# Kernel optimization log

Measured on AMD Instinct MI355X. Metric: run time of the kernel, lower is better.

The kernel has to match this reference:

```python
import jax, jax.numpy as jnp
import numpy as np


def setup_inputs() -> dict:
    key = jax.random.key(0)
    kq, kk, kv = jax.random.split(key, 3)
    B, S, D = 4, 4096, 128
    return {
        "q_proj": jax.random.normal(kq, (B, S, D), dtype=jnp.float32),
        "k_proj": jax.random.normal(kk, (B, S, D), dtype=jnp.float32),
        "v_proj": jax.random.normal(kv, (B, S, D), dtype=jnp.float32),
    }


def reference(q_proj, k_proj, v_proj):
    # Block-wise online softmax in the original is mathematically exact
    # full (non-causal) scaled dot-product attention.
    d = q_proj.shape[-1]
    scale = 1.0 / jnp.sqrt(jnp.asarray(d, dtype=q_proj.dtype))
    logits = jnp.einsum('bqd,bkd->bqk', q_proj, k_proj) * scale  # [B,S,S]
    attn = jax.nn.softmax(logits, axis=-1)
    return jnp.einsum('bqk,bkd->bqd', attn, v_proj)
```

## Files before the change

kernel.cpp:

```cpp
#include <hip/hip_runtime.h>
#include <hip/hip_bf16.h>
#include <stdint.h>

#define Bn 4
#define Sn 4096
#define Dn 128
#define SCALE ((float)(0.08838834764831843 * 1.4426950408889634))

typedef __attribute__((ext_vector_type(8)))  short short8;
typedef __attribute__((ext_vector_type(4)))  short short4v;
typedef __attribute__((ext_vector_type(4)))  float f32x4;
typedef __attribute__((ext_vector_type(16))) float f32x16;
typedef __attribute__((ext_vector_type(2)))  uint32_t uint2v;

__device__ __forceinline__ uint32_t bfround(float f){
  union { float f; uint32_t u; } a; a.f = f;
  return a.u + 0x7FFFu + ((a.u >> 16) & 1u);
}
__device__ __forceinline__ uint32_t f2bf2(float lo, float hi){
  return (bfround(hi) & 0xFFFF0000u) | (bfround(lo) >> 16);
}
__device__ __forceinline__ uint32_t f2bf2_fast(float lo, float hi){
  const uint32_t a = __float_as_uint(lo) + 0x8000u;
  const uint32_t b = __float_as_uint(hi) + 0x8000u;
  return __builtin_amdgcn_perm(b, a, 0x07060302u);
}
__device__ __forceinline__ float bf2f(short s){
  union { uint32_t u; float f; } a; a.u = ((uint32_t)(unsigned short)s) << 16; return a.f;
}
__device__ __forceinline__ float fexp2(float x){
#if __has_builtin(__builtin_amdgcn_exp2f)
  return __builtin_amdgcn_exp2f(x);
#else
  return exp2f(x);
#endif
}

__global__ void prep_kernel(const float* __restrict__ k, const float* __restrict__ v,
                            short* __restrict__ kb, short* __restrict__ vf){
  const int bid = blockIdx.x;
  const int t   = threadIdx.x;
  if (bid < 512){
    const int b = bid >> 7, i = bid & 127;
#pragma unroll
    for (int it=0; it<2; ++it){
      const int lin = it*256 + t;
      const int ln = lin & 31;
      const int tg = lin >> 5;
      const int tt = tg >> 1, hh = tg & 1;
      const float* src = k + ((size_t)(b*Sn + i*32 + ln))*Dn + tg*8;
      const f32x4 a = *(const f32x4*)src;
      const f32x4 c = *(const f32x4*)(src + 4);
      union { uint32_t u[4]; short8 s; } pk;
      pk.u[0] = f2bf2(a[0], a[1]);
      pk.u[1] = f2bf2(a[2], a[3]);
      pk.u[2] = f2bf2(c[0], c[1]);
      pk.u[3] = f2bf2(c[2], c[3]);
      *(short8*)(kb + (((size_t)(b*128 + i)*8 + tt)*64 + (hh*32 + ln))*8) = pk.s;
    }
  } else {
    __shared__ float tile[32][132];
    const int vb = bid - 512;
    const int b = vb >> 7, i = vb & 127;
#pragma unroll
    for (int it=0; it<4; ++it){
      const int lin = it*256 + t;
      const int row = lin >> 5;
      const int c4  = lin & 31;
      const f32x4 val = *(const f32x4*)(v + ((size_t)(b*Sn + i*32 + row))*Dn + c4*4);
      tile[row][c4*4+0] = val[0];
      tile[row][c4*4+1] = val[1];
      tile[row][c4*4+2] = val[2];
      tile[row][c4*4+3] = val[3];
    }
    __syncthreads();
#pragma unroll
    for (int cc=0; cc<2; ++cc){
      const int c = cc*256 + t;
      const int l = c & 63, fidx = c >> 6;
      const int t_ = fidx >> 2, mt = fidx & 3;
      const int ln = l & 31, h5 = l >> 5;
      const int d = mt*32 + ln;
      const int kb0 = 16*t_ + 4*h5;
      union { uint32_t u[4]; short8 s; } pk;
#pragma unroll
      for (int p=0;p<4;++p){
        const int j0 = 2*p, j1 = 2*p+1;
        const int kl0 = kb0 + (j0&3) + 8*(j0>>2);
        const int kl1 = kb0 + (j1&3) + 8*(j1>>2);
        pk.u[p] = f2bf2(tile[kl0][d], tile[kl1][d]);
      }
      *(short8*)(vf + (((size_t)(b*128 + i)*8 + fidx)*64 + l)*8) = pk.s;
    }
  }
}

__global__ __launch_bounds__(256, 2) void fa_kernel(
    const float* __restrict__ Qg, const short* __restrict__ Kb,
    const short* __restrict__ VFb, short* __restrict__ parts,
    float* __restrict__ lparts){
  const int tid = threadIdx.x;
  const int w = tid >> 6, lane = tid & 63;
  const int ln = lane & 31, h5 = lane >> 5;
  const int idx = blockIdx.x;
  const int b   = idx & 3;
  const int u2  = idx >> 2;
  const int qt  = u2 & 31;
  const int ks  = u2 >> 5;
  const int q0  = qt * 128;
  const int start_it = ks * 32;
  const int n_it     = 32;

  short8 Qf[8];
  {
    const float* qp = Qg + ((size_t)(b*Sn + q0 + w*32 + ln))*Dn;
#pragma unroll
    for (int t=0;t<8;++t){
      const int d0 = t*16 + h5*8;
      const f32x4 a = *(const f32x4*)(qp + d0);
      const f32x4 c = *(const f32x4*)(qp + d0 + 4);
      union { uint32_t u[4]; short8 s; } pk;
      pk.u[0] = f2bf2(a[0]*SCALE, a[1]*SCALE);
      pk.u[1] = f2bf2(a[2]*SCALE, a[3]*SCALE);
      pk.u[2] = f2bf2(c[0]*SCALE, c[1]*SCALE);
      pk.u[3] = f2bf2(c[2]*SCALE, c[3]*SCALE);
      Qf[t] = pk.s;
    }
  }

  f32x16 Ot[4];
#pragma unroll
  for (int m=0;m<4;++m)
#pragma unroll
    for (int r=0;r<16;++r) Ot[m][r] = 0.0f;
  float ls0=0.f, ls1=0.f, ls2=0.f, ls3=0.f;

  const short* Kbase = Kb  + (size_t)(b*128 + start_it)*4096 + (size_t)lane*8;
  const short* Vbase = VFb + (size_t)(b*128 + start_it)*4096 + (size_t)lane*8;

  short8 kf[8], vf[8];
  {
#pragma unroll
    for (int t=0;t<8;++t) kf[t] = *(const short8*)(Kbase + t*512);
#pragma unroll
    for (int t=0;t<8;++t) vf[t] = *(const short8*)(Vbase + t*512);
  }

  for (int i=0; i<n_it; ++i){
    f32x16 St;
#pragma unroll
    for (int r=0;r<16;++r) St[r] = 0.0f;
    __builtin_amdgcn_s_setprio(1);
#pragma unroll
    for (int t=0;t<8;++t)
      St = __builtin_amdgcn_mfma_f32_32x32x16_bf16(kf[t], Qf[t], St, 0, 0, 0);
    __builtin_amdgcn_s_setprio(0);

    {
      const short* Kp = Kbase + (size_t)(i+1)*4096;
#pragma unroll
      for (int t=0;t<8;++t) kf[t] = *(const short8*)(Kp + t*512);
    }
    __builtin_amdgcn_sched_barrier(0);

#pragma unroll
    for (int r=0;r<16;++r) St[r] = fexp2(St[r]);
#pragma unroll
    for (int r=0;r<16;r+=4){
      ls0 += St[r]; ls1 += St[r+1]; ls2 += St[r+2]; ls3 += St[r+3];
    }

    union { uint32_t u[4]; short8 s; } pf0, pf1;
    pf0.u[0] = f2bf2_fast(St[0], St[1]);
    pf0.u[1] = f2bf2_fast(St[2], St[3]);
    pf0.u[2] = f2bf2_fast(St[4], St[5]);
    pf0.u[3] = f2bf2_fast(St[6], St[7]);
    pf1.u[0] = f2bf2_fast(St[8], St[9]);
    pf1.u[1] = f2bf2_fast(St[10], St[11]);
    pf1.u[2] = f2bf2_fast(St[12], St[13]);
    pf1.u[3] = f2bf2_fast(St[14], St[15]);

    __builtin_amdgcn_s_setprio(1);
#pragma unroll
    for (int mt=0;mt<4;++mt)
      Ot[mt] = __builtin_amdgcn_mfma_f32_32x32x16_bf16(vf[mt],   pf0.s, Ot[mt], 0, 0, 0);
#pragma unroll
    for (int mt=0;mt<4;++mt)
      Ot[mt] = __builtin_amdgcn_mfma_f32_32x32x16_bf16(vf[4+mt], pf1.s, Ot[mt], 0, 0, 0);
    __builtin_amdgcn_s_setprio(0);

    {
      const short* Vp = Vbase + (size_t)(i+1)*4096;
#pragma unroll
      for (int t=0;t<8;++t) vf[t] = *(const short8*)(Vp + t*512);
    }
    __builtin_amdgcn_sched_barrier(0);
  }

  float lsum = (ls0 + ls1) + (ls2 + ls3);
  lsum += __shfl_xor(lsum, 32, 64);

  const int pslot = (b*32 + qt)*4 + ks;
  short* pbase = parts + (size_t)pslot*16384 + (size_t)(w*32 + ln)*128;
#pragma unroll
  for (int mt=0;mt<4;++mt){
#pragma unroll
    for (int g=0;g<4;++g){
      union { uint32_t u[2]; short4v s; } o;
      o.u[0] = f2bf2(Ot[mt][4*g],   Ot[mt][4*g+1]);
      o.u[1] = f2bf2(Ot[mt][4*g+2], Ot[mt][4*g+3]);
      *(short4v*)(pbase + mt*32 + 8*g + 4*h5) = o.s;
    }
  }
  if (h5 == 0) lparts[(size_t)pslot*128 + w*32 + ln] = lsum;
}

__global__ void reduce_kernel(const short* __restrict__ parts,
                              const float* __restrict__ lparts,
                              float* __restrict__ out){
  const int t  = threadIdx.x;
  const int s  = blockIdx.x >> 3;
  const int qg = (blockIdx.x & 7)*16 + (t >> 4);
  const int d0 = (t & 15) * 8;
  float acc[8];
#pragma unroll
  for (int j=0;j<8;++j) acc[j] = 0.0f;
  float lsum = 0.0f;
#pragma unroll
  for (int ks=0;ks<4;++ks){
    const short8 p = *(const short8*)(parts + ((size_t)(s*4+ks))*16384 + (size_t)qg*128 + d0);
#pragma unroll
    for (int j=0;j<8;++j) acc[j] += bf2f(p[j]);
    lsum += lparts[(size_t)(s*4+ks)*128 + qg];
  }
  const float linv = 1.0f / lsum;
  f32x4 o0, o1;
#pragma unroll
  for (int j=0;j<4;++j){ o0[j] = acc[j]*linv; o1[j] = acc[4+j]*linv; }
  float* op = out + ((size_t)(s*128 + qg))*128 + d0;
  *(f32x4*)op = o0;
  *(f32x4*)(op + 4) = o1;
}

extern "C" void kernel_launch(void* const* d_in, const int* in_sizes, int n_in,
                              void* d_out, int out_size, void* d_ws, size_t ws_size,
                              hipStream_t stream){
  const float* q = (const float*)d_in[0];
  const float* k = (const float*)d_in[1];
  const float* v = (const float*)d_in[2];
  float* out = (float*)d_out;
  char* ws = (char*)d_ws;
  short* kb     = (short*)ws;
  short* vfb    = kb + (size_t)Bn*Sn*Dn;
  short* parts  = (short*)(ws + 8388608);
  float* lparts = (float*)(ws + 8388608 + 16777216);

  prep_kernel<<<1024, 256, 0, stream>>>(k, v, kb, vfb);
  fa_kernel<<<512, 256, 0, stream>>>(q, kb, vfb, parts, lparts);
  reduce_kernel<<<1024, 256, 0, stream>>>(parts, lparts, out);
}
```

Measured before the change: 122.7 us.

## Software-pipeline QK^T MFMA one tile ahead of exp and PV

Restructures the attention loop so the QK^T scores for the next key tile are computed while the current tile's exponentials and PV MFMAs run, using two ping-ponged score accumulators. It also adds a prologue and epilogue, removes the sched_barrier and setprio hints, and prefetches K two tiles ahead. The aim is to overlap transcendental VALU work with matrix-core work within a wave. The cost is a second 16-float accumulator, which raises register pressure at 2 waves per SIMD, and the compiler's scheduling may now differ.

```diff
diff --git a/kernel.cpp b/kernel.cpp
--- a/kernel.cpp
+++ b/kernel.cpp
@@ -109,7 +109,6 @@
   const int ks  = u2 >> 5;
   const int q0  = qt * 128;
   const int start_it = ks * 32;
-  const int n_it     = 32;
 
   short8 Qf[8];
   {
@@ -135,66 +134,93 @@
     for (int r=0;r<16;++r) Ot[m][r] = 0.0f;
   float ls0=0.f, ls1=0.f, ls2=0.f, ls3=0.f;
 
+  f32x16 Zv;
+#pragma unroll
+  for (int r=0;r<16;++r) Zv[r] = 0.0f;
+
   const short* Kbase = Kb  + (size_t)(b*128 + start_it)*4096 + (size_t)lane*8;
   const short* Vbase = VFb + (size_t)(b*128 + start_it)*4096 + (size_t)lane*8;
 
   short8 kf[8], vf[8];
-  {
-#pragma unroll
-    for (int t=0;t<8;++t) kf[t] = *(const short8*)(Kbase + t*512);
-#pragma unroll
-    for (int t=0;t<8;++t) vf[t] = *(const short8*)(Vbase + t*512);
-  }
-
-  for (int i=0; i<n_it; ++i){
-    f32x16 St;
-#pragma unroll
-    for (int r=0;r<16;++r) St[r] = 0.0f;
-    __builtin_amdgcn_s_setprio(1);
-#pragma unroll
-    for (int t=0;t<8;++t)
-      St = __builtin_amdgcn_mfma_f32_32x32x16_bf16(kf[t], Qf[t], St, 0, 0, 0);
-    __builtin_amdgcn_s_setprio(0);
-
+#pragma unroll
+  for (int t=0;t<8;++t) kf[t] = *(const short8*)(Kbase + t*512);
+#pragma unroll
+  for (int t=0;t<8;++t) vf[t] = *(const short8*)(Vbase + t*512);
+
+  f32x16 StA, StB;
+  StA = __builtin_amdgcn_mfma_f32_32x32x16_bf16(kf[0], Qf[0], Zv, 0, 0, 0);
+#pragma unroll
+  for (int t=1;t<8;++t)
+    StA = __builtin_amdgcn_mfma_f32_32x32x16_bf16(kf[t], Qf[t], StA, 0, 0, 0);
+#pragma unroll
+  for (int t=0;t<8;++t) kf[t] = *(const short8*)(Kbase + 4096 + t*512);
+
+  auto body = [&](int i, f32x16& Scur, f32x16& Snx) {
+    Snx = __builtin_amdgcn_mfma_f32_32x32x16_bf16(kf[0], Qf[0], Zv, 0, 0, 0);
+#pragma unroll
+    for (int t=1;t<8;++t)
+      Snx = __builtin_amdgcn_mfma_f32_32x32x16_bf16(kf[t], Qf[t], Snx, 0, 0, 0);
     {
-      const short* Kp = Kbase + (size_t)(i+1)*4096;
+      const short* Kp = Kbase + (size_t)(i+2)*4096;
 #pragma unroll
       for (int t=0;t<8;++t) kf[t] = *(const short8*)(Kp + t*512);
     }
-    __builtin_amdgcn_sched_barrier(0);
-
-#pragma unroll
-    for (int r=0;r<16;++r) St[r] = fexp2(St[r]);
+#pragma unroll
+    for (int r=0;r<16;++r) Scur[r] = fexp2(Scur[r]);
 #pragma unroll
     for (int r=0;r<16;r+=4){
-      ls0 += St[r]; ls1 += St[r+1]; ls2 += St[r+2]; ls3 += St[r+3];
-    }
-
+      ls0 += Scur[r]; ls1 += Scur[r+1]; ls2 += Scur[r+2]; ls3 += Scur[r+3];
+    }
     union { uint32_t u[4]; short8 s; } pf0, pf1;
-    pf0.u[0] = f2bf2_fast(St[0], St[1]);
-    pf0.u[1] = f2bf2_fast(St[2], St[3]);
-    pf0.u[2] = f2bf2_fast(St[4], St[5]);
-    pf0.u[3] = f2bf2_fast(St[6], St[7]);
-    pf1.u[0] = f2bf2_fast(St[8], St[9]);
-    pf1.u[1] = f2bf2_fast(St[10], St[11]);
-    pf1.u[2] = f2bf2_fast(St[12], St[13]);
-    pf1.u[3] = f2bf2_fast(St[14], St[15]);
-
-    __builtin_amdgcn_s_setprio(1);
+    pf0.u[0] = f2bf2_fast(Scur[0],  Scur[1]);
+    pf0.u[1] = f2bf2_fast(Scur[2],  Scur[3]);
+    pf0.u[2] = f2bf2_fast(Scur[4],  Scur[5]);
+    pf0.u[3] = f2bf2_fast(Scur[6],  Scur[7]);
+    pf1.u[0] = f2bf2_fast(Scur[8],  Scur[9]);
+    pf1.u[1] = f2bf2_fast(Scur[10], Scur[11]);
+    pf1.u[2] = f2bf2_fast(Scur[12], Scur[13]);
+    pf1.u[3] = f2bf2_fast(Scur[14], Scur[15]);
 #pragma unroll
     for (int mt=0;mt<4;++mt)
       Ot[mt] = __builtin_amdgcn_mfma_f32_32x32x16_bf16(vf[mt],   pf0.s, Ot[mt], 0, 0, 0);
 #pragma unroll
     for (int mt=0;mt<4;++mt)
       Ot[mt] = __builtin_amdgcn_mfma_f32_32x32x16_bf16(vf[4+mt], pf1.s, Ot[mt], 0, 0, 0);
-    __builtin_amdgcn_s_setprio(0);
-
     {
       const short* Vp = Vbase + (size_t)(i+1)*4096;
 #pragma unroll
       for (int t=0;t<8;++t) vf[t] = *(const short8*)(Vp + t*512);
     }
-    __builtin_amdgcn_sched_barrier(0);
+  };
+
+  for (int i=0; i<30; i+=2){
+    body(i,   StA, StB);
+    body(i+1, StB, StA);
+  }
+  body(30, StA, StB);
+
+  {
+#pragma unroll
+    for (int r=0;r<16;++r) StB[r] = fexp2(StB[r]);
+#pragma unroll
+    for (int r=0;r<16;r+=4){
+      ls0 += StB[r]; ls1 += StB[r+1]; ls2 += StB[r+2]; ls3 += StB[r+3];
+    }
+    union { uint32_t u[4]; short8 s; } pf0, pf1;
+    pf0.u[0] = f2bf2_fast(StB[0],  StB[1]);
+    pf0.u[1] = f2bf2_fast(StB[2],  StB[3]);
+    pf0.u[2] = f2bf2_fast(StB[4],  StB[5]);
+    pf0.u[3] = f2bf2_fast(StB[6],  StB[7]);
+    pf1.u[0] = f2bf2_fast(StB[8],  StB[9]);
+    pf1.u[1] = f2bf2_fast(StB[10], StB[11]);
+    pf1.u[2] = f2bf2_fast(StB[12], StB[13]);
+    pf1.u[3] = f2bf2_fast(StB[14], StB[15]);
+#pragma unroll
+    for (int mt=0;mt<4;++mt)
+      Ot[mt] = __builtin_amdgcn_mfma_f32_32x32x16_bf16(vf[mt],   pf0.s, Ot[mt], 0, 0, 0);
+#pragma unroll
+    for (int mt=0;mt<4;++mt)
+      Ot[mt] = __builtin_amdgcn_mfma_f32_32x32x16_bf16(vf[4+mt], pf1.s, Ot[mt], 0, 0, 0);
   }
 
   float lsum = (ls0 + ls1) + (ls2 + ls3);
```

Result: no change. 124.1 us (+1.1%).

## Stage K/V tiles in LDS via async global-to-LDS loads, two Q tiles per wave

Applied to the files above, without the earlier changes.

Each block now has two waves, and each wave owns two 32-row Q tiles. The waves cooperatively stream K and V blocks into double-buffered shared memory with global_load_lds, so each K/V fragment is read from LDS once and reused across two MFMA accumulators. The key dimension is split six ways instead of four (768 blocks), and the reduce kernel and workspace offsets are updated to match. This cuts per-wave global K/V traffic and raises MFMA density per load. In exchange it adds a __syncthreads per iteration, more accumulator registers, and uneven split lengths.

```diff
diff --git a/kernel.cpp b/kernel.cpp
--- a/kernel.cpp
+++ b/kernel.cpp
@@ -34,6 +34,12 @@
 #else
   return exp2f(x);
 #endif
+}
+
+__device__ __forceinline__ void gload16(const void* g, void* l){
+  __builtin_amdgcn_global_load_lds(
+      (const __attribute__((address_space(1))) unsigned int*)g,
+      (__attribute__((address_space(3))) unsigned int*)l, 16, 0, 0);
 }
 
 __global__ void prep_kernel(const float* __restrict__ k, const float* __restrict__ v,
@@ -95,10 +101,11 @@
   }
 }
 
-__global__ __launch_bounds__(256, 2) void fa_kernel(
+__global__ __launch_bounds__(128, 2) void fa_kernel(
     const float* __restrict__ Qg, const short* __restrict__ Kb,
     const short* __restrict__ VFb, short* __restrict__ parts,
     float* __restrict__ lparts){
+  __shared__ __align__(16) char lds[32768];
   const int tid = threadIdx.x;
   const int w = tid >> 6, lane = tid & 63;
   const int ln = lane & 31, h5 = lane >> 5;
@@ -108,12 +115,13 @@
   const int qt  = u2 & 31;
   const int ks  = u2 >> 5;
   const int q0  = qt * 128;
-  const int start_it = ks * 32;
-  const int n_it     = 32;
-
-  short8 Qf[8];
-  {
-    const float* qp = Qg + ((size_t)(b*Sn + q0 + w*32 + ln))*Dn;
+  const int start_it = ks*21 + (ks < 2 ? ks : 2);
+  const int n_it     = 21 + (ks < 2 ? 1 : 0);
+
+  short8 Qf[2][8];
+#pragma unroll
+  for (int tile=0;tile<2;++tile){
+    const float* qp = Qg + ((size_t)(b*Sn + q0 + w*64 + tile*32 + ln))*Dn;
 #pragma unroll
     for (int t=0;t<8;++t){
       const int d0 = t*16 + h5*8;
@@ -124,95 +132,108 @@
       pk.u[1] = f2bf2(a[2]*SCALE, a[3]*SCALE);
       pk.u[2] = f2bf2(c[0]*SCALE, c[1]*SCALE);
       pk.u[3] = f2bf2(c[2]*SCALE, c[3]*SCALE);
-      Qf[t] = pk.s;
-    }
-  }
-
-  f32x16 Ot[4];
-#pragma unroll
-  for (int m=0;m<4;++m)
-#pragma unroll
-    for (int r=0;r<16;++r) Ot[m][r] = 0.0f;
-  float ls0=0.f, ls1=0.f, ls2=0.f, ls3=0.f;
-
-  const short* Kbase = Kb  + (size_t)(b*128 + start_it)*4096 + (size_t)lane*8;
-  const short* Vbase = VFb + (size_t)(b*128 + start_it)*4096 + (size_t)lane*8;
-
-  short8 kf[8], vf[8];
-  {
-#pragma unroll
-    for (int t=0;t<8;++t) kf[t] = *(const short8*)(Kbase + t*512);
-#pragma unroll
-    for (int t=0;t<8;++t) vf[t] = *(const short8*)(Vbase + t*512);
-  }
+      Qf[tile][t] = pk.s;
+    }
+  }
+
+  f32x16 Ot[2][4];
+#pragma unroll
+  for (int tile=0;tile<2;++tile)
+#pragma unroll
+    for (int m=0;m<4;++m)
+#pragma unroll
+      for (int r=0;r<16;++r) Ot[tile][m][r] = 0.0f;
+  float ls00=0.f, ls01=0.f, ls10=0.f, ls11=0.f;
+
+  const char* gsrc0 = (w ? (const char*)VFb : (const char*)Kb)
+                    + (size_t)(b*128)*8192 + (size_t)lane*16;
+  auto stage = [&](int it, int ph){
+    char* dst = lds + ph*16384 + (w ? 8192 : 0);
+    const char* src = gsrc0 + (size_t)it*8192;
+#pragma unroll
+    for (int u=0;u<8;++u) gload16(src + u*1024, dst + u*1024);
+  };
+
+  stage(start_it, 0);
 
   for (int i=0; i<n_it; ++i){
-    f32x16 St;
-#pragma unroll
-    for (int r=0;r<16;++r) St[r] = 0.0f;
+    const int ph = i & 1;
+    __syncthreads();
+    if (i+1 < n_it) stage(start_it+i+1, ph^1);
+
+    const char* bK = lds + ph*16384 + (size_t)lane*16;
+    const char* bV = bK + 8192;
+
+    f32x16 St0, St1;
+#pragma unroll
+    for (int r=0;r<16;++r){ St0[r] = 0.0f; St1[r] = 0.0f; }
     __builtin_amdgcn_s_setprio(1);
 #pragma unroll
-    for (int t=0;t<8;++t)
-      St = __builtin_amdgcn_mfma_f32_32x32x16_bf16(kf[t], Qf[t], St, 0, 0, 0);
+    for (int t=0;t<8;++t){
+      const short8 kf = *(const short8*)(bK + t*1024);
+      St0 = __builtin_amdgcn_mfma_f32_32x32x16_bf16(kf, Qf[0][t], St0, 0, 0, 0);
+      St1 = __builtin_amdgcn_mfma_f32_32x32x16_bf16(kf, Qf[1][t], St1, 0, 0, 0);
+    }
     __builtin_amdgcn_s_setprio(0);
 
-    {
-      const short* Kp = Kbase + (size_t)(i+1)*4096;
-#pragma unroll
-      for (int t=0;t<8;++t) kf[t] = *(const short8*)(Kp + t*512);
-    }
-    __builtin_amdgcn_sched_barrier(0);
-
-#pragma unroll
-    for (int r=0;r<16;++r) St[r] = fexp2(St[r]);
-#pragma unroll
-    for (int r=0;r<16;r+=4){
-      ls0 += St[r]; ls1 += St[r+1]; ls2 += St[r+2]; ls3 += St[r+3];
-    }
-
-    union { uint32_t u[4]; short8 s; } pf0, pf1;
-    pf0.u[0] = f2bf2_fast(St[0], St[1]);
-    pf0.u[1] = f2bf2_fast(St[2], St[3]);
-    pf0.u[2] = f2bf2_fast(St[4], St[5]);
-    pf0.u[3] = f2bf2_fast(St[6], St[7]);
-    pf1.u[0] = f2bf2_fast(St[8], St[9]);
-    pf1.u[1] = f2bf2_fast(St[10], St[11]);
-    pf1.u[2] = f2bf2_fast(St[12], St[13]);
-    pf1.u[3] = f2bf2_fast(St[14], St[15]);
+#pragma unroll
+    for (int r=0;r<16;++r) St0[r] = fexp2(St0[r]);
+#pragma unroll
+    for (int r=0;r<16;++r) St1[r] = fexp2(St1[r]);
+#pragma unroll
+    for (int r=0;r<16;r+=2){
+      ls00 += St0[r]; ls01 += St0[r+1];
+      ls10 += St1[r]; ls11 += St1[r+1];
+    }
+
+    union { uint32_t u[4]; short8 s; } pfA[2], pfB[2];
+#pragma unroll
+    for (int t=0;t<2;++t){
+      pfA[t].u[0] = f2bf2_fast(St0[8*t+0], St0[8*t+1]);
+      pfA[t].u[1] = f2bf2_fast(St0[8*t+2], St0[8*t+3]);
+      pfA[t].u[2] = f2bf2_fast(St0[8*t+4], St0[8*t+5]);
+      pfA[t].u[3] = f2bf2_fast(St0[8*t+6], St0[8*t+7]);
+      pfB[t].u[0] = f2bf2_fast(St1[8*t+0], St1[8*t+1]);
+      pfB[t].u[1] = f2bf2_fast(St1[8*t+2], St1[8*t+3]);
+      pfB[t].u[2] = f2bf2_fast(St1[8*t+4], St1[8*t+5]);
+      pfB[t].u[3] = f2bf2_fast(St1[8*t+6], St1[8*t+7]);
+    }
 
     __builtin_amdgcn_s_setprio(1);
 #pragma unroll
-    for (int mt=0;mt<4;++mt)
-      Ot[mt] = __builtin_amdgcn_mfma_f32_32x32x16_bf16(vf[mt],   pf0.s, Ot[mt], 0, 0, 0);
-#pragma unroll
-    for (int mt=0;mt<4;++mt)
-      Ot[mt] = __builtin_amdgcn_mfma_f32_32x32x16_bf16(vf[4+mt], pf1.s, Ot[mt], 0, 0, 0);
+    for (int t=0;t<2;++t){
+#pragma unroll
+      for (int mt=0;mt<4;++mt){
+        const short8 vf = *(const short8*)(bV + (t*4+mt)*1024);
+        Ot[0][mt] = __builtin_amdgcn_mfma_f32_32x32x16_bf16(vf, pfA[t].s, Ot[0][mt], 0, 0, 0);
+        Ot[1][mt] = __builtin_amdgcn_mfma_f32_32x32x16_bf16(vf, pfB[t].s, Ot[1][mt], 0, 0, 0);
+      }
+    }
     __builtin_amdgcn_s_setprio(0);
-
-    {
-      const short* Vp = Vbase + (size_t)(i+1)*4096;
-#pragma unroll
-      for (int t=0;t<8;++t) vf[t] = *(const short8*)(Vp + t*512);
-    }
-    __builtin_amdgcn_sched_barrier(0);
-  }
-
-  float lsum = (ls0 + ls1) + (ls2 + ls3);
-  lsum += __shfl_xor(lsum, 32, 64);
-
-  const int pslot = (b*32 + qt)*4 + ks;
-  short* pbase = parts + (size_t)pslot*16384 + (size_t)(w*32 + ln)*128;
-#pragma unroll
-  for (int mt=0;mt<4;++mt){
-#pragma unroll
-    for (int g=0;g<4;++g){
-      union { uint32_t u[2]; short4v s; } o;
-      o.u[0] = f2bf2(Ot[mt][4*g],   Ot[mt][4*g+1]);
-      o.u[1] = f2bf2(Ot[mt][4*g+2], Ot[mt][4*g+3]);
-      *(short4v*)(pbase + mt*32 + 8*g + 4*h5) = o.s;
-    }
-  }
-  if (h5 == 0) lparts[(size_t)pslot*128 + w*32 + ln] = lsum;
+  }
+
+  float lsum0 = ls00 + ls01; lsum0 += __shfl_xor(lsum0, 32, 64);
+  float lsum1 = ls10 + ls11; lsum1 += __shfl_xor(lsum1, 32, 64);
+
+  const int pslot = (b*32 + qt)*6 + ks;
+#pragma unroll
+  for (int tile=0;tile<2;++tile){
+    short* pbase = parts + (size_t)pslot*16384 + (size_t)(w*64 + tile*32 + ln)*128;
+#pragma unroll
+    for (int mt=0;mt<4;++mt){
+#pragma unroll
+      for (int g=0;g<4;++g){
+        union { uint32_t u[2]; short4v s; } o;
+        o.u[0] = f2bf2(Ot[tile][mt][4*g],   Ot[tile][mt][4*g+1]);
+        o.u[1] = f2bf2(Ot[tile][mt][4*g+2], Ot[tile][mt][4*g+3]);
+        *(short4v*)(pbase + mt*32 + 8*g + 4*h5) = o.s;
+      }
+    }
+  }
+  if (h5 == 0){
+    lparts[(size_t)pslot*128 + w*64 + ln]      = lsum0;
+    lparts[(size_t)pslot*128 + w*64 + 32 + ln] = lsum1;
+  }
 }
 
 __global__ void reduce_kernel(const short* __restrict__ parts,
@@ -227,11 +248,11 @@
   for (int j=0;j<8;++j) acc[j] = 0.0f;
   float lsum = 0.0f;
 #pragma unroll
-  for (int ks=0;ks<4;++ks){
-    const short8 p = *(const short8*)(parts + ((size_t)(s*4+ks))*16384 + (size_t)qg*128 + d0);
+  for (int ks=0;ks<6;++ks){
+    const short8 p = *(const short8*)(parts + ((size_t)(s*6+ks))*16384 + (size_t)qg*128 + d0);
 #pragma unroll
     for (int j=0;j<8;++j) acc[j] += bf2f(p[j]);
-    lsum += lparts[(size_t)(s*4+ks)*128 + qg];
+    lsum += lparts[(size_t)(s*6+ks)*128 + qg];
   }
   const float linv = 1.0f / lsum;
   f32x4 o0, o1;
@@ -253,9 +274,9 @@
   short* kb     = (short*)ws;
   short* vfb    = kb + (size_t)Bn*Sn*Dn;
   short* parts  = (short*)(ws + 8388608);
-  float* lparts = (float*)(ws + 8388608 + 16777216);
+  float* lparts = (float*)(ws + 8388608 + 25165824);
 
   prep_kernel<<<1024, 256, 0, stream>>>(k, v, kb, vfb);
-  fa_kernel<<<512, 256, 0, stream>>>(q, kb, vfb, parts, lparts);
+  fa_kernel<<<768, 128, 0, stream>>>(q, kb, vfb, parts, lparts);
   reduce_kernel<<<1024, 256, 0, stream>>>(parts, lparts, out);
 }
```

Result: no change. 123.5 us (+0.6%).
